# Optimization experiments

Measured on AMD Instinct MI355X. Metric: run time of the kernel, lower is better.

## Reference

```python
import jax, jax.numpy as jnp
import numpy as np

EPS = 1e-6
NEG = -10000.0

def compute_alibi_slopes(n_head):
    # standard ALiBi slopes for power-of-two head counts: 2^{-8(i+1)/n}
    start = 2.0 ** (-8.0 / n_head)
    return jnp.asarray([start ** (i + 1) for i in range(n_head)], dtype=jnp.float32)

def setup_inputs() -> dict:
    key = jax.random.key(0)
    k1, k2, k3 = jax.random.split(key, 3)
    B, T, C, H = 2, 2048, 1024, 16
    x = jax.random.normal(k1, (B, T, C), dtype=jnp.float32)
    # torch nn.Linear weights are [out_features, in_features]
    w_qkv = jax.random.normal(k2, (3 * C, C), dtype=jnp.float32) * (C ** -0.5)
    w_out = jax.random.normal(k3, (C, C), dtype=jnp.float32) * (C ** -0.5)
    alibi_slopes = compute_alibi_slopes(H)
    return {"x": x, "w_qkv": w_qkv, "w_out": w_out, "alibi_slopes": alibi_slopes}

def rational_softmax(scores, eps=EPS):
    # algebraic sigmoid 0.5*(1 + x/sqrt(1+x^2)) normalized along last axis
    num = 0.5 * (1.0 + scores * jax.lax.rsqrt(1.0 + scores * scores))
    return num / (jnp.sum(num, axis=-1, keepdims=True) + eps)

def reference(x, w_qkv, w_out, alibi_slopes):
    B, T, C = x.shape
    H = alibi_slopes.shape[0]
    D = C // H
    scale = 1.0 / jnp.sqrt(jnp.float32(D))
    qkv = (x @ w_qkv.T).reshape(B, T, 3, H, D)
    qkv = jnp.transpose(qkv, (2, 0, 3, 1, 4))  # [3,B,H,T,D]
    q, k, v = qkv[0], qkv[1], qkv[2]
    scores = jnp.einsum("bhtd,bhsd->bhts", q, k) * scale  # [B,H,T,T]
    pos = jnp.arange(T)
    rel = pos[:, None] - pos[None, :]  # [T,T]
    alibi = -jnp.abs(rel).astype(jnp.float32) * alibi_slopes[None, :, None, None]
    scores = scores + alibi
    causal = rel < 0  # strictly upper triangle (j > i)
    scores = jnp.where(causal[None, None], NEG, scores)
    probs = rational_softmax(scores, EPS)
    out = jnp.einsum("bhts,bhsd->bhtd", probs, v)  # [B,H,T,D]
    out = jnp.transpose(out, (0, 2, 1, 3)).reshape(B, T, C)
    return out @ w_out.T
```

## Files before the change

kernel.cpp:

```cpp
#include <hip/hip_runtime.h>
#include <stdint.h>

typedef __attribute__((ext_vector_type(8))) short bf16x8;
typedef __attribute__((ext_vector_type(4))) float f32x4;
typedef __attribute__((ext_vector_type(16))) float f32x16;

#define MFMA_16x16x32(a, b, c) __builtin_amdgcn_mfma_f32_16x16x32_bf16((a), (b), (c), 0, 0, 0)
#define MFMA_32x32x16(a, b, c) __builtin_amdgcn_mfma_f32_32x32x16_bf16((a), (b), (c), 0, 0, 0)

__device__ __forceinline__ short f2bf(float f) {
  union { float f; uint32_t u; } x;
  x.f = f;
  uint32_t r = x.u + 0x7fffu + ((x.u >> 16) & 1u);
  return (short)(r >> 16);
}

__device__ __forceinline__ uint32_t cvt_pk_bf16(float lo, float hi) {
  uint32_t r;
  asm("v_cvt_pk_bf16_f32 %0, %1, %2" : "=v"(r) : "v"(lo), "v"(hi));
  return r;
}

__device__ __forceinline__ void gload_lds16(const short* g, short* l) {
  __builtin_amdgcn_global_load_lds(
      (const __attribute__((address_space(1))) void*)g,
      (__attribute__((address_space(3))) void*)l, 16, 0, 0);
}

__global__ __launch_bounds__(256) void cast_all(const float* __restrict__ x,
                                                const float* __restrict__ wq,
                                                const float* __restrict__ wo,
                                                short* __restrict__ xb,
                                                short* __restrict__ wqb,
                                                short* __restrict__ wob) {
  int i = blockIdx.x * 256 + threadIdx.x;
  const float* s;
  short* d;
  int off;
  float sc = 1.0f;
  if (i < 524288) { s = x; d = xb; off = i; }
  else if (i < 917504) {
    s = wq; d = wqb; off = i - 524288;
    if (off < 131072) sc = 0.125f;
  }
  else { s = wo; d = wob; off = i - 917504; }
  const float4* sp = (const float4*)s;
  float4 v0 = sp[(size_t)off * 2 + 0];
  float4 v1 = sp[(size_t)off * 2 + 1];
  bf16x8 o;
  o[0] = f2bf(v0.x * sc); o[1] = f2bf(v0.y * sc); o[2] = f2bf(v0.z * sc); o[3] = f2bf(v0.w * sc);
  o[4] = f2bf(v1.x * sc); o[5] = f2bf(v1.y * sc); o[6] = f2bf(v1.z * sc); o[7] = f2bf(v1.w * sc);
  *(bf16x8*)(d + (size_t)off * 8) = o;
}

template <int OUT_BF16>
__global__ __launch_bounds__(512, 2) void gemm256(const short* __restrict__ A,
                                                  const short* __restrict__ B,
                                                  void* __restrict__ Cp,
                                                  int M, int N, int K, int ntN) {
  __shared__ short Al[2][2][128 * 64];
  __shared__ short Bl[2][2][128 * 64];

  const int tid = threadIdx.x;
  const int wv = tid >> 6, lane = tid & 63;
  const int wr = wv >> 2, wc = wv & 3;
  const int lrow = lane & 15, kgrp = lane >> 4;
  const int l3 = lrow & 7;
  const int ck0 = ((kgrp ^ l3)) * 8;
  const int ck1 = ((kgrp ^ l3) ^ 4) * 8;

  const int nwg = gridDim.x;
  const int orig = blockIdx.x;
  const int wg = (orig & 7) * (nwg >> 3) + (orig >> 3);
  const int by = wg / ntN, bx = wg % ntN;
  const int row0 = by * 256, col0 = bx * 256;

  const int r_ = tid >> 3;
  const int cs_ = ((tid & 7) ^ (r_ & 7)) * 8;

  const int NT = K >> 6;
  const int NI = NT >> 1;
  const int NTm1 = NT - 1;

  auto stgA = [&](int slot, int h, int j, int kt) {
    gload_lds16(A + (size_t)(row0 + h * 128 + j * 64 + r_) * K + kt * 64 + cs_,
                &Al[slot][h][j * 4096 + wv * 512]);
  };
  auto stgB = [&](int slot, int h, int j, int kt) {
    gload_lds16(B + (size_t)(col0 + h * 128 + j * 64 + r_) * K + kt * 64 + cs_,
                &Bl[slot][h][j * 4096 + wv * 512]);
  };

  f32x4 acc[8][4] = {};

  const int boff = ((wc & 1) * 64 + lrow) * 64;
  const int bh = wc >> 1;

  stgB(0, 0, 0, 0); stgB(0, 0, 1, 0); stgB(0, 1, 0, 0); stgB(0, 1, 1, 0);
  stgA(0, 0, 0, 0); stgA(0, 0, 1, 0); stgA(0, 1, 0, 0); stgA(0, 1, 1, 0);
  stgB(1, 0, 0, 1); stgB(1, 0, 1, 1); stgB(1, 1, 0, 1); stgB(1, 1, 1, 1);
  asm volatile("s_waitcnt vmcnt(4)" ::: "memory");
  __builtin_amdgcn_s_barrier();

  for (int i = 0; i < NI; ++i) {
    const int ktB1 = (2 * i + 1);
    const int ktP2 = (2 * i + 2 > NTm1) ? NTm1 : 2 * i + 2;
    const int ktP3 = (2 * i + 3 > NTm1) ? NTm1 : 2 * i + 3;
#pragma unroll
    for (int s = 0; s < 2; ++s) {
      bf16x8 bfr[4][2];
#pragma unroll
      for (int q = 0; q < 4; ++q) {
        if (q == 0) {
#pragma unroll
          for (int n = 0; n < 4; ++n) {
            bfr[n][0] = *(const bf16x8*)(&Bl[s][bh][boff + n * 1024 + ck0]);
            bfr[n][1] = *(const bf16x8*)(&Bl[s][bh][boff + n * 1024 + ck1]);
          }
        }
        bf16x8 afr[2][2];
#pragma unroll
        for (int mm = 0; mm < 2; ++mm) {
          const int m = q * 2 + mm;
          afr[mm][0] = *(const bf16x8*)(&Al[s][wr][lrow * 64 + m * 1024 + ck0]);
          afr[mm][1] = *(const bf16x8*)(&Al[s][wr][lrow * 64 + m * 1024 + ck1]);
        }
        if (s == 0) {
          if (q == 0) { stgA(1, 0, 0, ktB1); stgA(1, 0, 1, ktB1); stgA(1, 1, 0, ktB1); stgA(1, 1, 1, ktB1); }
          else if (q == 1) { stgB(0, 0, 0, ktP2); stgB(0, 0, 1, ktP2); }
          else if (q == 2) { stgB(0, 1, 0, ktP2); stgB(0, 1, 1, ktP2); }
        } else {
          if (q == 0) { stgA(0, 0, 0, ktP2); stgA(0, 0, 1, ktP2); stgA(0, 1, 0, ktP2); stgA(0, 1, 1, ktP2); }
          else if (q == 1) { stgB(1, 0, 0, ktP3); stgB(1, 0, 1, ktP3); }
          else if (q == 2) { stgB(1, 1, 0, ktP3); stgB(1, 1, 1, ktP3); }
        }
        __builtin_amdgcn_sched_barrier(0);
        __builtin_amdgcn_s_barrier();
        asm volatile("s_waitcnt lgkmcnt(0)" ::: "memory");
        __builtin_amdgcn_sched_barrier(0);
        __builtin_amdgcn_s_setprio(1);
#pragma unroll
        for (int mm = 0; mm < 2; ++mm)
#pragma unroll
          for (int n = 0; n < 4; ++n)
#pragma unroll
            for (int kk = 0; kk < 2; ++kk)
              acc[q * 2 + mm][n] = MFMA_16x16x32(afr[mm][kk], bfr[n][kk], acc[q * 2 + mm][n]);
        __builtin_amdgcn_s_setprio(0);
        __builtin_amdgcn_sched_barrier(0);
        if (q == 3) {
          asm volatile("s_waitcnt vmcnt(4)" ::: "memory");
        }
        __builtin_amdgcn_s_barrier();
      }
    }
  }

  asm volatile("s_waitcnt vmcnt(0)" ::: "memory");

#pragma unroll
  for (int m = 0; m < 8; ++m) {
    const int grow = row0 + wr * 128 + m * 16 + kgrp * 4;
#pragma unroll
    for (int n = 0; n < 4; ++n) {
      const int gcol = col0 + wc * 64 + n * 16 + lrow;
#pragma unroll
      for (int j = 0; j < 4; ++j) {
        const size_t off = (size_t)(grow + j) * N + gcol;
        if (OUT_BF16) ((short*)Cp)[off] = f2bf(acc[m][n][j]);
        else          ((float*)Cp)[off] = acc[m][n][j];
      }
    }
  }
}

template <int OUT_BF16>
__global__ __launch_bounds__(256, 4) void gemm_bt64(const short* __restrict__ A,
                                                    const short* __restrict__ B,
                                                    void* __restrict__ Cp,
                                                    int M, int N, int K) {
  __shared__ short As[64 * 64];
  __shared__ short Bs[128 * 64];
  const int tid = threadIdx.x;
  const int wave = tid >> 6, lane = tid & 63;
  const int wr = wave >> 1, wc = wave & 1;
  const int row0 = blockIdx.y * 64, col0 = blockIdx.x * 128;
  const int lrow = lane & 15;
  const int kgrp = lane >> 4;
  const int l3 = lrow & 7;

  const int r_ = tid >> 3;
  const int cs_ = ((tid & 7) ^ (r_ & 7)) * 8;

  f32x4 acc[2][4] = {};

  for (int k0 = 0; k0 < K; k0 += 64) {
#pragma unroll
    for (int it = 0; it < 2; ++it)
      gload_lds16(A + (size_t)(row0 + it * 32 + r_) * K + k0 + cs_,
                  As + (it * 256 + wave * 64) * 8);
#pragma unroll
    for (int it = 0; it < 4; ++it)
      gload_lds16(B + (size_t)(col0 + it * 32 + r_) * K + k0 + cs_,
                  Bs + (it * 256 + wave * 64) * 8);
    __syncthreads();
#pragma unroll
    for (int kk = 0; kk < 2; ++kk) {
      const int ck = ((kk * 4 + kgrp) ^ l3) * 8;
      bf16x8 a[2], b[4];
#pragma unroll
      for (int m = 0; m < 2; ++m)
        a[m] = *(const bf16x8*)(As + (wr * 32 + m * 16 + lrow) * 64 + ck);
#pragma unroll
      for (int n = 0; n < 4; ++n)
        b[n] = *(const bf16x8*)(Bs + (wc * 64 + n * 16 + lrow) * 64 + ck);
#pragma unroll
      for (int m = 0; m < 2; ++m)
#pragma unroll
        for (int n = 0; n < 4; ++n)
          acc[m][n] = MFMA_16x16x32(a[m], b[n], acc[m][n]);
    }
    __syncthreads();
  }

#pragma unroll
  for (int m = 0; m < 2; ++m) {
    int rbase = row0 + wr * 32 + m * 16 + kgrp * 4;
#pragma unroll
    for (int n = 0; n < 4; ++n) {
      int col = col0 + wc * 64 + n * 16 + lrow;
#pragma unroll
      for (int j = 0; j < 4; ++j) {
        size_t off = (size_t)(rbase + j) * N + col;
        if (OUT_BF16) ((short*)Cp)[off] = f2bf(acc[m][n][j]);
        else          ((float*)Cp)[off] = acc[m][n][j];
      }
    }
  }
}

__global__ __launch_bounds__(256) void transpose_v(const short* __restrict__ qkv,
                                                   short* __restrict__ vt) {
  const int T = 2048;
  __shared__ short sm[64][72];
  const int bh = blockIdx.y, h = bh & 15, b = bh >> 4;
  const int t0 = blockIdx.x * 64;
  const int tid = threadIdx.x;
#pragma unroll
  for (int p = 0; p < 2; ++p) {
    int idx = p * 256 + tid;
    int tl = idx >> 3, d0 = (idx & 7) * 8;
    bf16x8 v = *(const bf16x8*)(qkv + (b * T + t0 + tl) * 3072 + 2048 + h * 64 + d0);
    *(bf16x8*)(&sm[tl][d0]) = v;
  }
  __syncthreads();
#pragma unroll
  for (int p = 0; p < 2; ++p) {
    int idx = p * 256 + tid;
    int d = idx >> 3, ts0 = (idx & 7) * 8;
    bf16x8 o;
#pragma unroll
    for (int j = 0; j < 8; ++j) o[j] = sm[ts0 + j][d];
    *(bf16x8*)(vt + (bh * 64 + d) * T + t0 + ts0) = o;
  }
}

template <bool DIAG>
__device__ __forceinline__ void attn_sub(
    const short* __restrict__ Kb, const short* __restrict__ Vb,
    const bf16x8 (&qf)[4], const f32x16& crun,
    f32x16& acc0, f32x16& acc1, float (&den4)[4],
    int l31, int hi, int shalf, int mbits) {
  const int krow = l31 >> 1;
  const int kc0 = (l31 & 1) * 8 + hi;
  const int ss = shalf;
  __builtin_amdgcn_s_setprio(1);
  const bf16x8 kf0 = *(const bf16x8*)(Kb + (ss * 16 + krow) * 128 + (kc0 ^ krow) * 8);
  f32x16 s = MFMA_32x32x16(kf0, qf[0], crun);
#pragma unroll
  for (int kkd = 1; kkd < 4; ++kkd) {
    const bf16x8 kf = *(const bf16x8*)(Kb + (ss * 16 + krow) * 128 +
                                       ((kc0 + kkd * 2) ^ krow) * 8);
    s = MFMA_32x32x16(kf, qf[kkd], s);
  }
  __builtin_amdgcn_s_setprio(0);
  float nm[16];
#pragma unroll
  for (int v = 0; v < 16; ++v) {
    float x = s[v];
    if (DIAG) x = ((mbits >> v) & 1) ? -10000.0f : x;
    float t = fmaf(x, x, 1.0f);
    float num = fmaf(x * __builtin_amdgcn_rsqf(t), 0.5f, 0.5f);
    den4[v & 3] += num;
    nm[v] = num;
  }
#pragma unroll
  for (int k1 = 0; k1 < 2; ++k1) {
    union { uint32_t u[4]; bf16x8 v8; } pu;
#pragma unroll
    for (int w01 = 0; w01 < 2; ++w01) {
      uint32_t c0 = cvt_pk_bf16(nm[2 * w01 + 8 * k1], nm[2 * w01 + 8 * k1 + 1]);
      uint32_t c1 = cvt_pk_bf16(nm[2 * w01 + 8 * k1 + 4], nm[2 * w01 + 8 * k1 + 5]);
      asm volatile("v_permlane32_swap_b32 %0, %1" : "+v"(c0), "+v"(c1));
      pu.u[w01] = c0;
      pu.u[w01 + 2] = c1;
    }
    const int vsw = ((((l31 & 1) * 8) + ss * 4 + k1 * 2 + hi) ^ krow) * 8;
    const bf16x8 vf0 = *(const bf16x8*)(Vb + krow * 128 + vsw);
    const bf16x8 vf1 = *(const bf16x8*)(Vb + (16 + krow) * 128 + vsw);
    __builtin_amdgcn_s_setprio(1);
    acc0 = MFMA_32x32x16(pu.v8, vf0, acc0);
    acc1 = MFMA_32x32x16(pu.v8, vf1, acc1);
    __builtin_amdgcn_s_setprio(0);
  }
}

__global__ __launch_bounds__(256, 4) void attn_kernel(const short* __restrict__ qkv,
                                                      const short* __restrict__ vt,
                                                      const float* __restrict__ slopes,
                                                      short* __restrict__ attn_out) {
  const int T = 2048, C = 1024, C3 = 3072;
  __shared__ short Kl[2][4096];
  __shared__ short Vl[2][4096];
  __shared__ float denm[64];

  const int tid = threadIdx.x, wv = tid >> 6, lane = tid & 63;
  const int l31 = lane & 31, hi = lane >> 5;
  const int wg = blockIdx.x;
  const int bh = (wg & 7) + ((wg >> 3) & 3) * 8;
  const int qi = 31 - (wg >> 5);
  const int b = bh >> 4, h = bh & 15;
  const int qsub = wv >> 1, shalf = wv & 1;
  const float slope = slopes[h];
  const float s64 = slope * 64.0f;

  const int W = (int)(45.0f / (64.0f * slope)) + 2;
  const int kt0 = (qi - W > 0) ? (qi - W) : 0;

  const int qg = qi * 64 + qsub * 32 + l31;
  bf16x8 qf[4];
#pragma unroll
  for (int ks = 0; ks < 4; ++ks)
    qf[ks] = *(const bf16x8*)(qkv + (size_t)(b * T + qg) * C3 + h * 64 + ks * 16 + hi * 8);

  f32x16 crun;
  int mbits = 0;
#pragma unroll
  for (int v = 0; v < 16; ++v) {
    int s32 = (v & 3) + 8 * (v >> 2) + 4 * hi;
    crun[v] = slope * (float)(s32 - l31 + 32 * (shalf - qsub) + 64 * (kt0 - qi));
    if (s32 > l31) mbits |= (1 << v);
  }

  int koff[2], voff[2];
#pragma unroll
  for (int p = 0; p < 2; ++p) {
    int idx = p * 256 + tid;
    int rho = idx >> 4, u = idx & 15, c = u ^ (rho & 15);
    koff[p] = (2 * rho + (c >> 3)) * C3 + (c & 7) * 8;
    voff[p] = (2 * rho + (c >> 3)) * T + (c & 7) * 8;
  }
  const short* kbase = qkv + (size_t)b * T * C3 + C + h * 64;
  const short* vbase = vt + (size_t)bh * 64 * T;

  auto STAGE = [&](int bufi, int kt) {
#pragma unroll
    for (int p = 0; p < 2; ++p)
      gload_lds16(kbase + (size_t)kt * 64 * C3 + koff[p], &Kl[bufi][(p * 256 + wv * 64) * 8]);
#pragma unroll
    for (int p = 0; p < 2; ++p)
      gload_lds16(vbase + kt * 64 + voff[p], &Vl[bufi][(p * 256 + wv * 64) * 8]);
  };

  f32x16 acc0 = {}, acc1 = {};
  float den4[4] = {0.f, 0.f, 0.f, 0.f};

  STAGE(0, kt0);
  asm volatile("s_waitcnt vmcnt(0)" ::: "memory");
  __builtin_amdgcn_s_barrier();
  int cur = 0;

  for (int kt = kt0; kt < qi; ++kt) {
    STAGE(cur ^ 1, kt + 1);
    attn_sub<false>(Kl[cur], Vl[cur], qf, crun, acc0, acc1, den4, l31, hi, shalf, mbits);
#pragma unroll
    for (int v = 0; v < 16; ++v) crun[v] += s64;
    asm volatile("s_waitcnt vmcnt(0)" ::: "memory");
    __builtin_amdgcn_s_barrier();
    cur ^= 1;
  }
  if (!(qsub == 0 && shalf == 1)) {
    if (qsub == 1 && shalf == 0)
      attn_sub<false>(Kl[cur], Vl[cur], qf, crun, acc0, acc1, den4, l31, hi, shalf, mbits);
    else
      attn_sub<true>(Kl[cur], Vl[cur], qf, crun, acc0, acc1, den4, l31, hi, shalf, mbits);
  }
  __syncthreads();

  float den = (den4[0] + den4[1]) + (den4[2] + den4[3]);
  den += __shfl_xor(den, 32);

  if (shalf == 1) {
    float* mp = (float*)(qsub == 0 ? &Kl[cur ^ 1][0] : &Vl[cur ^ 1][0]);
#pragma unroll
    for (int i = 0; i < 16; ++i) {
      mp[i * 64 + lane] = acc0[i];
      mp[(16 + i) * 64 + lane] = acc1[i];
    }
    if (hi == 0) denm[qsub * 32 + l31] = den;
  }
  __syncthreads();

  if (shalf == 0) {
    const float* mp = (const float*)(qsub == 0 ? &Kl[cur ^ 1][0] : &Vl[cur ^ 1][0]);
    den += denm[qsub * 32 + l31];
#pragma unroll
    for (int i = 0; i < 16; ++i) {
      acc0[i] += mp[i * 64 + lane];
      acc1[i] += mp[(16 + i) * 64 + lane];
    }
    short* obase = attn_out + (size_t)(b * T + qi * 64 + qsub * 32) * C + h * 64;
#pragma unroll
    for (int v = 0; v < 16; ++v) {
      int ql = (v & 3) + 8 * (v >> 2) + 4 * hi;
      float dv = __int_as_float(__builtin_amdgcn_ds_bpermute(ql << 2, __float_as_int(den)));
      float r = __builtin_amdgcn_rcpf(dv + 1e-6f);
      obase[(size_t)ql * C + l31] = f2bf(acc0[v] * r);
      obase[(size_t)ql * C + 32 + l31] = f2bf(acc1[v] * r);
    }
  }
}

extern "C" void kernel_launch(void* const* d_in, const int* in_sizes, int n_in,
                              void* d_out, int out_size, void* d_ws, size_t ws_size,
                              hipStream_t stream) {
  const float* x      = (const float*)d_in[0];
  const float* w_qkv  = (const float*)d_in[1];
  const float* w_out  = (const float*)d_in[2];
  const float* slopes = (const float*)d_in[3];

  const int B = 2, T = 2048, C = 1024;
  const int M = B * T;
  const int N1 = 3 * C;

  char* ws = (char*)d_ws;
  short* x_bf    = (short*)(ws);
  short* wqkv_bf = (short*)(ws + 8388608);
  short* wout_bf = (short*)(ws + 14680064);
  short* qkv_bf  = (short*)(ws + 16777216);
  short* vt_bf   = (short*)(ws + 41943040);
  short* ao_bf   = (short*)(ws + 50331648);

  cast_all<<<4096, 256, 0, stream>>>(x, w_qkv, w_out, x_bf, wqkv_bf, wout_bf);

  gemm256<1><<<dim3((M / 256) * (N1 / 256)), 512, 0, stream>>>(x_bf, wqkv_bf, qkv_bf,
                                                               M, N1, C, N1 / 256);

  transpose_v<<<dim3(T / 64, 32), 256, 0, stream>>>(qkv_bf, vt_bf);

  attn_kernel<<<1024, 256, 0, stream>>>(qkv_bf, vt_bf, slopes, ao_bf);

  gemm_bt64<0><<<dim3(C / 128, M / 64), 256, 0, stream>>>(ao_bf, wout_bf, (float*)d_out, M, C, C);
}
```

Baseline: 107.8 us.

## Schedule attention tiles dynamically via a global atomic work counter

The attention kernel now pulls (head, query-tile) work items from a global atomic counter in a loop, instead of mapping each block statically to one tile. The counter is reset inside the V-transpose kernel and lives in workspace space that held the bf16 copy of x, which is no longer needed at that point. The goal is to balance the very uneven per-tile cost from the causal ALiBi window across CUs. In exchange it adds an atomic and an extra barrier per item. The launch bound also drops from 4 to 3 blocks per CU, which changes register budget and occupancy.

```diff
diff --git a/kernel.cpp b/kernel.cpp
--- a/kernel.cpp
+++ b/kernel.cpp
@@ -240,12 +240,14 @@
 }
 
 __global__ __launch_bounds__(256) void transpose_v(const short* __restrict__ qkv,
-                                                   short* __restrict__ vt) {
+                                                   short* __restrict__ vt,
+                                                   int* __restrict__ wcnt) {
   const int T = 2048;
   __shared__ short sm[64][72];
   const int bh = blockIdx.y, h = bh & 15, b = bh >> 4;
   const int t0 = blockIdx.x * 64;
   const int tid = threadIdx.x;
+  if (blockIdx.x == 0 && blockIdx.y == 0 && tid == 0) *wcnt = 0;
 #pragma unroll
   for (int p = 0; p < 2; ++p) {
     int idx = p * 256 + tid;
@@ -315,43 +317,27 @@
   }
 }
 
-__global__ __launch_bounds__(256, 4) void attn_kernel(const short* __restrict__ qkv,
+__global__ __launch_bounds__(256, 3) void attn_kernel(const short* __restrict__ qkv,
                                                       const short* __restrict__ vt,
                                                       const float* __restrict__ slopes,
-                                                      short* __restrict__ attn_out) {
+                                                      short* __restrict__ attn_out,
+                                                      int* __restrict__ wcnt) {
   const int T = 2048, C = 1024, C3 = 3072;
   __shared__ short Kl[2][4096];
   __shared__ short Vl[2][4096];
   __shared__ float denm[64];
+  __shared__ int itemS;
 
   const int tid = threadIdx.x, wv = tid >> 6, lane = tid & 63;
   const int l31 = lane & 31, hi = lane >> 5;
-  const int wg = blockIdx.x;
-  const int bh = (wg & 7) + ((wg >> 3) & 3) * 8;
-  const int qi = 31 - (wg >> 5);
-  const int b = bh >> 4, h = bh & 15;
   const int qsub = wv >> 1, shalf = wv & 1;
-  const float slope = slopes[h];
-  const float s64 = slope * 64.0f;
-
-  const int W = (int)(45.0f / (64.0f * slope)) + 2;
-  const int kt0 = (qi - W > 0) ? (qi - W) : 0;
-
-  const int qg = qi * 64 + qsub * 32 + l31;
-  bf16x8 qf[4];
-#pragma unroll
-  for (int ks = 0; ks < 4; ++ks)
-    qf[ks] = *(const bf16x8*)(qkv + (size_t)(b * T + qg) * C3 + h * 64 + ks * 16 + hi * 8);
-
-  f32x16 crun;
+
   int mbits = 0;
 #pragma unroll
   for (int v = 0; v < 16; ++v) {
     int s32 = (v & 3) + 8 * (v >> 2) + 4 * hi;
-    crun[v] = slope * (float)(s32 - l31 + 32 * (shalf - qsub) + 64 * (kt0 - qi));
     if (s32 > l31) mbits |= (1 << v);
   }
-
   int koff[2], voff[2];
 #pragma unroll
   for (int p = 0; p < 2; ++p) {
@@ -360,74 +346,113 @@
     koff[p] = (2 * rho + (c >> 3)) * C3 + (c & 7) * 8;
     voff[p] = (2 * rho + (c >> 3)) * T + (c & 7) * 8;
   }
-  const short* kbase = qkv + (size_t)b * T * C3 + C + h * 64;
-  const short* vbase = vt + (size_t)bh * 64 * T;
-
-  auto STAGE = [&](int bufi, int kt) {
-#pragma unroll
-    for (int p = 0; p < 2; ++p)
-      gload_lds16(kbase + (size_t)kt * 64 * C3 + koff[p], &Kl[bufi][(p * 256 + wv * 64) * 8]);
-#pragma unroll
-    for (int p = 0; p < 2; ++p)
-      gload_lds16(vbase + kt * 64 + voff[p], &Vl[bufi][(p * 256 + wv * 64) * 8]);
-  };
-
-  f32x16 acc0 = {}, acc1 = {};
-  float den4[4] = {0.f, 0.f, 0.f, 0.f};
-
-  STAGE(0, kt0);
-  asm volatile("s_waitcnt vmcnt(0)" ::: "memory");
-  __builtin_amdgcn_s_barrier();
-  int cur = 0;
-
-  for (int kt = kt0; kt < qi; ++kt) {
-    STAGE(cur ^ 1, kt + 1);
-    attn_sub<false>(Kl[cur], Vl[cur], qf, crun, acc0, acc1, den4, l31, hi, shalf, mbits);
-#pragma unroll
-    for (int v = 0; v < 16; ++v) crun[v] += s64;
+
+  while (true) {
+    if (tid == 0) itemS = atomicAdd(wcnt, 1);
+    __syncthreads();
+    const int item = itemS;
+    if (item >= 1024) break;
+
+    const int bh = item & 31;
+    const int qi = 31 - (item >> 5);
+    const int b = bh >> 4, h = bh & 15;
+    const float slope = slopes[h];
+    const float s64 = slope * 64.0f;
+
+    const int W = (int)(45.0f / (64.0f * slope)) + 2;
+    const int kt0 = (qi - W > 0) ? (qi - W) : 0;
+
+    const short* kbase = qkv + (size_t)b * T * C3 + C + h * 64;
+    const short* vbase = vt + (size_t)bh * 64 * T;
+
+    {
+#pragma unroll
+      for (int p = 0; p < 2; ++p)
+        gload_lds16(kbase + (size_t)kt0 * 64 * C3 + koff[p], &Kl[0][(p * 256 + wv * 64) * 8]);
+#pragma unroll
+      for (int p = 0; p < 2; ++p)
+        gload_lds16(vbase + kt0 * 64 + voff[p], &Vl[0][(p * 256 + wv * 64) * 8]);
+    }
+
+    const int qg = qi * 64 + qsub * 32 + l31;
+    bf16x8 qf[4];
+#pragma unroll
+    for (int ks = 0; ks < 4; ++ks)
+      qf[ks] = *(const bf16x8*)(qkv + (size_t)(b * T + qg) * C3 + h * 64 + ks * 16 + hi * 8);
+
+    f32x16 crun;
+#pragma unroll
+    for (int v = 0; v < 16; ++v) {
+      int s32 = (v & 3) + 8 * (v >> 2) + 4 * hi;
+      crun[v] = slope * (float)(s32 - l31 + 32 * (shalf - qsub) + 64 * (kt0 - qi));
+    }
+
+    f32x16 acc0 = {}, acc1 = {};
+    float den4[4] = {0.f, 0.f, 0.f, 0.f};
+
     asm volatile("s_waitcnt vmcnt(0)" ::: "memory");
     __builtin_amdgcn_s_barrier();
-    cur ^= 1;
-  }
-  if (!(qsub == 0 && shalf == 1)) {
-    if (qsub == 1 && shalf == 0)
+    int cur = 0;
+
+    for (int kt = kt0; kt < qi; ++kt) {
+      {
+        const int kt1 = kt + 1;
+#pragma unroll
+        for (int p = 0; p < 2; ++p)
+          gload_lds16(kbase + (size_t)kt1 * 64 * C3 + koff[p],
+                      &Kl[cur ^ 1][(p * 256 + wv * 64) * 8]);
+#pragma unroll
+        for (int p = 0; p < 2; ++p)
+          gload_lds16(vbase + kt1 * 64 + voff[p], &Vl[cur ^ 1][(p * 256 + wv * 64) * 8]);
+      }
       attn_sub<false>(Kl[cur], Vl[cur], qf, crun, acc0, acc1, den4, l31, hi, shalf, mbits);
-    else
-      attn_sub<true>(Kl[cur], Vl[cur], qf, crun, acc0, acc1, den4, l31, hi, shalf, mbits);
-  }
-  __syncthreads();
-
-  float den = (den4[0] + den4[1]) + (den4[2] + den4[3]);
-  den += __shfl_xor(den, 32);
-
-  if (shalf == 1) {
-    float* mp = (float*)(qsub == 0 ? &Kl[cur ^ 1][0] : &Vl[cur ^ 1][0]);
-#pragma unroll
-    for (int i = 0; i < 16; ++i) {
-      mp[i * 64 + lane] = acc0[i];
-      mp[(16 + i) * 64 + lane] = acc1[i];
-    }
-    if (hi == 0) denm[qsub * 32 + l31] = den;
-  }
-  __syncthreads();
-
-  if (shalf == 0) {
-    const float* mp = (const float*)(qsub == 0 ? &Kl[cur ^ 1][0] : &Vl[cur ^ 1][0]);
-    den += denm[qsub * 32 + l31];
-#pragma unroll
-    for (int i = 0; i < 16; ++i) {
-      acc0[i] += mp[i * 64 + lane];
-      acc1[i] += mp[(16 + i) * 64 + lane];
-    }
-    short* obase = attn_out + (size_t)(b * T + qi * 64 + qsub * 32) * C + h * 64;
-#pragma unroll
-    for (int v = 0; v < 16; ++v) {
-      int ql = (v & 3) + 8 * (v >> 2) + 4 * hi;
-      float dv = __int_as_float(__builtin_amdgcn_ds_bpermute(ql << 2, __float_as_int(den)));
-      float r = __builtin_amdgcn_rcpf(dv + 1e-6f);
-      obase[(size_t)ql * C + l31] = f2bf(acc0[v] * r);
-      obase[(size_t)ql * C + 32 + l31] = f2bf(acc1[v] * r);
-    }
+#pragma unroll
+      for (int v = 0; v < 16; ++v) crun[v] += s64;
+      asm volatile("s_waitcnt vmcnt(0)" ::: "memory");
+      __builtin_amdgcn_s_barrier();
+      cur ^= 1;
+    }
+    if (!(qsub == 0 && shalf == 1)) {
+      if (qsub == 1 && shalf == 0)
+        attn_sub<false>(Kl[cur], Vl[cur], qf, crun, acc0, acc1, den4, l31, hi, shalf, mbits);
+      else
+        attn_sub<true>(Kl[cur], Vl[cur], qf, crun, acc0, acc1, den4, l31, hi, shalf, mbits);
+    }
+    __syncthreads();
+
+    float den = (den4[0] + den4[1]) + (den4[2] + den4[3]);
+    den += __shfl_xor(den, 32);
+
+    if (shalf == 1) {
+      float* mp = (float*)(qsub == 0 ? &Kl[cur ^ 1][0] : &Vl[cur ^ 1][0]);
+#pragma unroll
+      for (int i = 0; i < 16; ++i) {
+        mp[i * 64 + lane] = acc0[i];
+        mp[(16 + i) * 64 + lane] = acc1[i];
+      }
+      if (hi == 0) denm[qsub * 32 + l31] = den;
+    }
+    __syncthreads();
+
+    if (shalf == 0) {
+      const float* mp = (const float*)(qsub == 0 ? &Kl[cur ^ 1][0] : &Vl[cur ^ 1][0]);
+      den += denm[qsub * 32 + l31];
+#pragma unroll
+      for (int i = 0; i < 16; ++i) {
+        acc0[i] += mp[i * 64 + lane];
+        acc1[i] += mp[(16 + i) * 64 + lane];
+      }
+      short* obase = attn_out + (size_t)(b * T + qi * 64 + qsub * 32) * C + h * 64;
+#pragma unroll
+      for (int v = 0; v < 16; ++v) {
+        int ql = (v & 3) + 8 * (v >> 2) + 4 * hi;
+        float dv = __int_as_float(__builtin_amdgcn_ds_bpermute(ql << 2, __float_as_int(den)));
+        float r = __builtin_amdgcn_rcpf(dv + 1e-6f);
+        obase[(size_t)ql * C + l31] = f2bf(acc0[v] * r);
+        obase[(size_t)ql * C + 32 + l31] = f2bf(acc1[v] * r);
+      }
+    }
+    __syncthreads();
   }
 }
 
@@ -450,15 +475,16 @@
   short* qkv_bf  = (short*)(ws + 16777216);
   short* vt_bf   = (short*)(ws + 41943040);
   short* ao_bf   = (short*)(ws + 50331648);
+  int*   wcnt    = (int*)(ws);
 
   cast_all<<<4096, 256, 0, stream>>>(x, w_qkv, w_out, x_bf, wqkv_bf, wout_bf);
 
   gemm256<1><<<dim3((M / 256) * (N1 / 256)), 512, 0, stream>>>(x_bf, wqkv_bf, qkv_bf,
                                                                M, N1, C, N1 / 256);
 
-  transpose_v<<<dim3(T / 64, 32), 256, 0, stream>>>(qkv_bf, vt_bf);
-
-  attn_kernel<<<1024, 256, 0, stream>>>(qkv_bf, vt_bf, slopes, ao_bf);
+  transpose_v<<<dim3(T / 64, 32), 256, 0, stream>>>(qkv_bf, vt_bf, wcnt);
+
+  attn_kernel<<<1024, 256, 0, stream>>>(qkv_bf, vt_bf, slopes, ao_bf, wcnt);
 
   gemm_bt64<0><<<dim3(C / 128, M / 64), 256, 0, stream>>>(ao_bf, wout_bf, (float*)d_out, M, C, C);
 }
```

Measured after the change: 117.2 us. 1.09x slower.
